# Performance work log

Measured on AMD Instinct MI355X. Metric: run time of the kernel, lower is better.

Reference implementation:

```python
import jax, jax.numpy as jnp
import numpy as np

H = 1024
B, S = 4, 2048
SCALE = 1.0 / np.sqrt(H)  # single-head: head_dim == hidden_dim


def setup_inputs() -> dict:
    key = jax.random.key(0)
    k1, k2, k3, k4 = jax.random.split(key, 4)
    inp = jax.random.normal(k1, (B, S, H), dtype=jnp.float32)
    # nn.Linear(h, h, bias=False) weights, stored [out, in]
    wq = jax.random.normal(k2, (H, H), dtype=jnp.float32) / np.sqrt(H)
    wk = jax.random.normal(k3, (H, H), dtype=jnp.float32) / np.sqrt(H)
    wv = jax.random.normal(k4, (H, H), dtype=jnp.float32) / np.sqrt(H)
    # causal mask, broadcast over batch: 1 = attend, 0 = masked
    attention_mask = jnp.broadcast_to(
        jnp.tril(jnp.ones((S, S), dtype=jnp.int32)), (B, S, S))
    return {"input": inp, "attention_mask": attention_mask,
            "wq": wq, "wk": wk, "wv": wv}


def reference(input, attention_mask, wq, wk, wv):
    # Linear: x @ W^T
    Q = jnp.einsum('bsh,oh->bso', input, wq)
    K = jnp.einsum('bsh,oh->bso', input, wk)
    V = jnp.einsum('bsh,oh->bso', input, wv)
    scores = jnp.einsum('bqh,bkh->bqk', Q, K) * SCALE  # [B,S,S]
    neg_inf = jnp.asarray(-jnp.inf, dtype=scores.dtype)
    scores = jnp.where(attention_mask == 0, neg_inf, scores)
    attn = jax.nn.softmax(scores, axis=-1)
    # dropout prob = 0.0 (eval): identity
    return jnp.einsum('bqk,bkh->bqh', attn, V)
```

## Files before the change

### kernel.cpp

```cpp
#include <hip/hip_runtime.h>
#include <hip/hip_bf16.h>
#include <stdint.h>

typedef __attribute__((ext_vector_type(8))) short short8;
typedef __attribute__((ext_vector_type(4))) float f32x4;
typedef __attribute__((ext_vector_type(4))) float fvec4;
typedef __attribute__((ext_vector_type(4))) unsigned short us4;

#define DEV static __device__ __forceinline__

constexpr int Hn = 1024;
constexpr int Bn = 4;
constexpr int Sn = 2048;
constexpr float SCALE_F = 0.03125f;
constexpr float LOG2E_F = 1.4426950408889634f;
constexpr float CEXP = SCALE_F * LOG2E_F;
constexpr int PTILES = 136;

DEV unsigned short f2bf(float f) {
  union { float f; unsigned u; } c; c.f = f;
  unsigned r = c.u + 0x7fffu + ((c.u >> 16) & 1u);
  return (unsigned short)(r >> 16);
}

DEV void gload16(const void* g, void* l) {
  __builtin_amdgcn_global_load_lds(
      (const __attribute__((address_space(1))) void*)g,
      (__attribute__((address_space(3))) void*)l, 16, 0, 0);
}

#define VMCNT(n) asm volatile("s_waitcnt vmcnt(" #n ")" ::: "memory")
#define LGKM0()  asm volatile("s_waitcnt lgkmcnt(0)" ::: "memory")
#define BAR()    asm volatile("s_barrier" ::: "memory")

DEV int swz_wg(int bid, int n) {
  const int q = n >> 3, r = n & 7, x = bid & 7, o = bid >> 3;
  return (x < r ? x * (q + 1) : r * (q + 1) + (x - r) * q) + o;
}

__global__ __launch_bounds__(256) void cvt_kernel(
    const float* __restrict__ x, const float* __restrict__ wq,
    const float* __restrict__ wk, const float* __restrict__ wv,
    unsigned short* __restrict__ xb, unsigned short* __restrict__ wb,
    float* __restrict__ lz) {
  if (blockIdx.x == 0) {
    f32x4 z = {0.f, 0.f, 0.f, 0.f};
    for (int i = threadIdx.x; i < Bn * Sn / 4; i += 256) ((f32x4*)lz)[i] = z;
  }
  const int NX4 = Bn * Sn * Hn / 4;
  const int NW4 = Hn * Hn / 4;
  const int total = NX4 + 3 * NW4;
  for (int i = blockIdx.x * 256 + threadIdx.x; i < total; i += gridDim.x * 256) {
    const fvec4* s; us4* d; int j;
    if (i < NX4)                { s = (const fvec4*)x;  d = (us4*)xb;             j = i; }
    else if (i < NX4 + NW4)     { s = (const fvec4*)wq; d = (us4*)wb;             j = i - NX4; }
    else if (i < NX4 + 2 * NW4) { s = (const fvec4*)wk; d = (us4*)(wb + Hn * Hn); j = i - NX4 - NW4; }
    else                        { s = (const fvec4*)wv; d = (us4*)(wb + 2 * Hn * Hn); j = i - NX4 - 2 * NW4; }
    fvec4 v = s[j];
    us4 o;
    o[0] = f2bf(v[0]); o[1] = f2bf(v[1]); o[2] = f2bf(v[2]); o[3] = f2bf(v[3]);
    d[j] = o;
  }
}

#define MFMA16(H, V, B) do {                                                     \
  __builtin_amdgcn_s_setprio(1);                                                 \
  _Pragma("unroll") for (int m_ = 0; m_ < 4; m_++)                               \
  _Pragma("unroll") for (int n_ = 0; n_ < 2; n_++)                               \
  _Pragma("unroll") for (int ks_ = 0; ks_ < 2; ks_++)                            \
    acc[H][V][m_][n_] = __builtin_amdgcn_mfma_f32_16x16x32_bf16(                 \
        afr[m_][ks_], (B)[n_][ks_], acc[H][V][m_][n_], 0, 0, 0);                 \
  __builtin_amdgcn_s_setprio(0);                                                 \
  __builtin_amdgcn_sched_barrier(0);                                             \
} while (0)

template <int MODE>
__global__ __launch_bounds__(512, 2) void gemm256_kernel(
    const unsigned short* __restrict__ A, int lda, int64_t a_bstride,
    const unsigned short* __restrict__ Bm, int ldb, int64_t b_bstride,
    unsigned short* __restrict__ C0, unsigned short* __restrict__ C1,
    float* __restrict__ lsum, int n_split, int ldc, int bm_mod, int K) {
  __shared__ __attribute__((aligned(16))) unsigned short LDSm[8][8192];
  char* lds = (char*)LDSm;
  const int tid = threadIdx.x, lane = tid & 63, wave = tid >> 6;
  const int wr = wave >> 2, wc = wave & 3;
  const int ln15 = lane & 15, hi = lane >> 4;

  int bm, bn, zl = 0;
  const int wg = swz_wg(blockIdx.x, gridDim.x);
  if (MODE == 0) { bm = wg % bm_mod; bn = wg / bm_mod; }
  else {
    zl = wg / 36;
    const int t = wg - zl * 36;
    bm = (int)((sqrtf(8.f * t + 1.f) - 1.f) * 0.5f);
    if (bm * (bm + 1) / 2 > t) bm--;
    if ((bm + 1) * (bm + 2) / 2 <= t) bm++;
    bn = t - bm * (bm + 1) / 2;
  }
  const unsigned short* Ab = A + (int64_t)zl * a_bstride;
  const unsigned short* Bb = Bm + (int64_t)zl * b_bstride;

  const int srow = tid >> 3;
  const int kch = ((tid & 7) ^ (srow & 7)) << 3;
  const unsigned short* Ag = Ab + (int64_t)(bm * 256 + srow) * lda + kch;
  const unsigned short* Bg = Bb + (int64_t)(bn * 256 + srow) * ldb + kch;
  const int dst_off = tid * 16;

  auto stageA = [&](int half, int t, int buf) {
    const unsigned short* s = Ag + (int64_t)(half * 128) * lda + (t << 6);
    char* d = lds + ((buf * 4 + half) << 14) + dst_off;
    gload16(s, d);
    gload16(s + (int64_t)64 * lda, d + 8192);
  };
  auto stageB = [&](int half, int t, int buf) {
    const unsigned short* s = Bg + (int64_t)(half * 128) * ldb + (t << 6);
    char* d = lds + ((buf * 4 + 2 + half) << 14) + dst_off;
    gload16(s, d);
    gload16(s + (int64_t)64 * ldb, d + 8192);
  };
  auto rdA = [&](int buf, int half, int rr, int ks) -> short8 {
    return *(const short8*)(lds + ((buf * 4 + half) << 14) + rr * 128 +
                            (((ks << 6) + (hi << 4)) ^ ((rr & 7) << 4)));
  };
  auto rdB = [&](int buf, int half, int rr, int ks) -> short8 {
    return *(const short8*)(lds + ((buf * 4 + 2 + half) << 14) + rr * 128 +
                            (((ks << 6) + (hi << 4)) ^ ((rr & 7) << 4)));
  };

  f32x4 acc[2][2][4][2];
#pragma unroll
  for (int h = 0; h < 2; h++)
#pragma unroll
    for (int v = 0; v < 2; v++)
#pragma unroll
      for (int m = 0; m < 4; m++)
#pragma unroll
        for (int n = 0; n < 2; n++) acc[h][v][m][n] = (f32x4){0.f, 0.f, 0.f, 0.f};

  short8 afr[4][2], b0r[2][2], b1r[2][2];

  stageA(0, 0, 0); stageB(0, 0, 0); stageB(1, 0, 0); stageA(1, 0, 0);
  VMCNT(4);
  BAR();

  const int nkt = K >> 6;
  for (int t = 0; t < nkt; ++t) {
    const int buf = t & 1, nb2 = buf ^ 1;
    const bool st = (t + 1 < nkt);
#pragma unroll
    for (int m = 0; m < 4; m++) {
      afr[m][0] = rdA(buf, 0, wr * 64 + m * 16 + ln15, 0);
      afr[m][1] = rdA(buf, 0, wr * 64 + m * 16 + ln15, 1);
    }
#pragma unroll
    for (int n = 0; n < 2; n++) {
      b0r[n][0] = rdB(buf, 0, wc * 32 + n * 16 + ln15, 0);
      b0r[n][1] = rdB(buf, 0, wc * 32 + n * 16 + ln15, 1);
    }
    if (st) { stageA(0, t + 1, nb2); VMCNT(4); } else { VMCNT(2); }
    BAR(); LGKM0(); __builtin_amdgcn_sched_barrier(0);
    MFMA16(0, 0, b0r);
    BAR();
#pragma unroll
    for (int n = 0; n < 2; n++) {
      b1r[n][0] = rdB(buf, 1, wc * 32 + n * 16 + ln15, 0);
      b1r[n][1] = rdB(buf, 1, wc * 32 + n * 16 + ln15, 1);
    }
    if (st) { stageB(0, t + 1, nb2); VMCNT(4); } else { VMCNT(0); }
    BAR(); LGKM0(); __builtin_amdgcn_sched_barrier(0);
    MFMA16(0, 1, b1r);
    BAR();
#pragma unroll
    for (int m = 0; m < 4; m++) {
      afr[m][0] = rdA(buf, 1, wr * 64 + m * 16 + ln15, 0);
      afr[m][1] = rdA(buf, 1, wr * 64 + m * 16 + ln15, 1);
    }
    if (st) { stageB(1, t + 1, nb2); VMCNT(6); } else { VMCNT(0); }
    BAR(); LGKM0(); __builtin_amdgcn_sched_barrier(0);
    MFMA16(1, 0, b0r);
    BAR();
    if (st) { stageA(1, t + 1, nb2); VMCNT(4); } else { VMCNT(0); }
    BAR();
    MFMA16(1, 1, b1r);
    BAR();
  }

  if (MODE == 0) {
#pragma unroll
    for (int h = 0; h < 2; h++)
#pragma unroll
      for (int v = 0; v < 2; v++)
#pragma unroll
        for (int n = 0; n < 2; n++) {
          int cc = bn * 256 + v * 128 + wc * 32 + n * 16;
          unsigned short* cb = C0;
          if (cc >= n_split) { cb = C1; cc -= n_split; }
          cc += ln15;
#pragma unroll
          for (int m = 0; m < 4; m++) {
            const int r0 = bm * 256 + h * 128 + wr * 64 + m * 16 + hi * 4;
#pragma unroll
            for (int j = 0; j < 4; j++)
              cb[(int64_t)(r0 + j) * ldc + cc] = f2bf(acc[h][v][m][n][j]);
          }
        }
  } else {
    unsigned short* Pb = C0 + (int64_t)zl * (PTILES * 16384);
    float* lb = lsum + zl * Sn;
#pragma unroll
    for (int h = 0; h < 2; h++)
#pragma unroll
      for (int m = 0; m < 4; m++)
#pragma unroll
        for (int j = 0; j < 4; j++) {
          const int row = bm * 256 + h * 128 + wr * 64 + m * 16 + hi * 4 + j;
          const int tq = row >> 7;
          float s = 0.f;
#pragma unroll
          for (int v = 0; v < 2; v++)
#pragma unroll
            for (int n = 0; n < 2; n++) {
              const int col = bn * 256 + v * 128 + wc * 32 + n * 16 + ln15;
              const float p =
                  (col <= row) ? __builtin_amdgcn_exp2f(acc[h][v][m][n][j] * CEXP) : 0.f;
              s += p;
              const int tk = col >> 7;
              if (tk <= tq)
                Pb[((int64_t)(tq * (tq + 1) / 2 + tk) << 14) + ((row & 127) << 7) +
                   (col & 127)] = f2bf(p);
            }
          s += __shfl_xor(s, 1); s += __shfl_xor(s, 2);
          s += __shfl_xor(s, 4); s += __shfl_xor(s, 8);
          if (ln15 == 0) atomicAdd(&lb[row], s);
        }
  }
}

__global__ __launch_bounds__(256, 2) void pv_gemm_kernel(
    const unsigned short* __restrict__ Pp,
    const unsigned short* __restrict__ VTb,
    const float* __restrict__ l,
    float* __restrict__ Out) {
  const int xcd = blockIdx.x & 7;
  const int inner = blockIdx.x >> 3;
  const int bn = inner & 7;
  const int slot = inner >> 3;
  const int r = slot * 8 + xcd;
  const int bm = 15 - (r >> 2);
  const int b = r & 3;

  __shared__ __attribute__((aligned(16))) unsigned short As[2][128 * 64];
  __shared__ __attribute__((aligned(16))) unsigned short Bs[2][128 * 64];
  const int tid = threadIdx.x, lane = tid & 63, wave = tid >> 6;
  const int wr = wave >> 1, wc = wave & 1;
  const int ln15 = lane & 15, hi = lane >> 4;

  const int srow0 = wave * 8 + (lane >> 3);
  const int gch = (((lane & 7) ^ (srow0 & 7)) << 3);
  const unsigned short* Pbase = Pp + (int64_t)b * (PTILES * 16384) +
      ((int64_t)(bm * (bm + 1) / 2) << 14);
  const unsigned short* Vbase = VTb + (int64_t)(bn * 128) * (Bn * Sn) + (int64_t)b * Sn;

  auto stage = [&](int kt, int buf) {
    char* a = (char*)As[buf] + wave * 1024;
    char* bl = (char*)Bs[buf] + wave * 1024;
    const int64_t a_off = ((int64_t)(kt >> 1) << 14) + (kt & 1) * 64 + gch;
    const int64_t v_off = (int64_t)kt * 64 + gch;
#pragma unroll
    for (int j = 0; j < 4; ++j) {
      const int row = srow0 + j * 32;
      gload16(Pbase + a_off + ((int64_t)row << 7), a + j * 4096);
      gload16(Vbase + v_off + (int64_t)row * (Bn * Sn), bl + j * 4096);
    }
  };

  f32x4 acc[4][4];
#pragma unroll
  for (int m = 0; m < 4; m++)
#pragma unroll
    for (int n = 0; n < 4; n++) acc[m][n] = (f32x4){0.f, 0.f, 0.f, 0.f};

  const int nkt = (bm + 1) * 2;
  stage(0, 0);
  for (int kt = 0; kt < nkt; ++kt) {
    const int buf = kt & 1;
    if (kt + 1 < nkt) { stage(kt + 1, buf ^ 1); VMCNT(8); }
    else { VMCNT(0); }
    BAR();
    const char* Ap = (const char*)As[buf];
    const char* Bp = (const char*)Bs[buf];
    short8 af[4][2], bf[4][2];
#pragma unroll
    for (int m = 0; m < 4; m++) {
      const int rr = wr * 64 + m * 16 + ln15;
#pragma unroll
      for (int ks = 0; ks < 2; ks++)
        af[m][ks] = *(const short8*)(Ap + rr * 128 + (((ks << 6) + (hi << 4)) ^ ((rr & 7) << 4)));
    }
#pragma unroll
    for (int n = 0; n < 4; n++) {
      const int rr = wc * 64 + n * 16 + ln15;
#pragma unroll
      for (int ks = 0; ks < 2; ks++)
        bf[n][ks] = *(const short8*)(Bp + rr * 128 + (((ks << 6) + (hi << 4)) ^ ((rr & 7) << 4)));
    }
#pragma unroll
    for (int ks = 0; ks < 2; ks++)
#pragma unroll
      for (int m = 0; m < 4; m++)
#pragma unroll
        for (int n = 0; n < 4; n++)
          acc[m][n] = __builtin_amdgcn_mfma_f32_16x16x32_bf16(af[m][ks], bf[n][ks], acc[m][n], 0, 0, 0);
    BAR();
  }

#pragma unroll
  for (int m = 0; m < 4; m++) {
    const int r0 = bm * 128 + wr * 64 + m * 16 + hi * 4;
#pragma unroll
    for (int j = 0; j < 4; j++) {
      const int q = r0 + j;
      const float linv = 1.0f / l[(int64_t)b * Sn + q];
#pragma unroll
      for (int n = 0; n < 4; n++) {
        const int d = bn * 128 + wc * 64 + n * 16 + ln15;
        Out[(int64_t)b * Sn * Hn + (int64_t)q * Hn + d] = acc[m][n][j] * linv;
      }
    }
  }
}

extern "C" void kernel_launch(void* const* d_in, const int* in_sizes, int n_in,
                              void* d_out, int out_size, void* d_ws, size_t ws_size,
                              hipStream_t stream) {
  const float* x  = (const float*)d_in[0];
  const float* wq = (const float*)d_in[2];
  const float* wk = (const float*)d_in[3];
  const float* wv = (const float*)d_in[4];
  float* out = (float*)d_out;
  char* ws = (char*)d_ws;

  const int64_t MiB = 1ll << 20;
  unsigned short* xb = (unsigned short*)(ws);
  unsigned short* wb = (unsigned short*)(ws + 16 * MiB);
  unsigned short* Pp = (unsigned short*)(ws);
  float* l           = (float*)(ws + 22 * MiB);
  unsigned short* Qb = (unsigned short*)(ws + 23 * MiB);
  unsigned short* Kb = (unsigned short*)(ws + 39 * MiB);
  unsigned short* VT = (unsigned short*)(ws + 55 * MiB);

  cvt_kernel<<<2048, 256, 0, stream>>>(x, wq, wk, wv, xb, wb, l);
  gemm256_kernel<0><<<256, 512, 0, stream>>>(
      xb, 1024, 0, wb, 1024, 0, Qb, Kb, nullptr, 1024, 1024, 32, 1024);
  gemm256_kernel<0><<<128, 512, 0, stream>>>(
      wb + 2 * 1024 * 1024, 1024, 0, xb, 1024, 0, VT, VT, nullptr, 1 << 30, 8192, 4, 1024);
  gemm256_kernel<1><<<144, 512, 0, stream>>>(
      Qb, 1024, (int64_t)Sn * Hn, Kb, 1024, (int64_t)Sn * Hn,
      Pp, nullptr, l, 1 << 30, 0, 0, 1024);
  pv_gemm_kernel<<<512, 256, 0, stream>>>(Pp, VT, l, out);
}
```

Measured before the change: 158.9 us.

## Use 128x128 tile GEMM kernel for V projection and causal QK^T scores

Adds a new 256-thread gemm128 kernel with simple double buffering and moves the V^T projection and the causal QK^T/exp stage onto it. The QK^T stage now launches one block per lower-triangular 128x128 tile (544 blocks) instead of 144 blocks on 256x256 tiles. This cuts wasted work above the diagonal and raises parallelism on the 256-CU part. In exchange it gives up the tuned 256-tile ping-pong pipeline and gets less operand reuse per block. The gemm256 kernel is reduced to the Q/K projection path only.

```diff
diff --git a/kernel.cpp b/kernel.cpp
--- a/kernel.cpp
+++ b/kernel.cpp
@@ -74,36 +74,24 @@
   __builtin_amdgcn_sched_barrier(0);                                             \
 } while (0)
 
-template <int MODE>
 __global__ __launch_bounds__(512, 2) void gemm256_kernel(
-    const unsigned short* __restrict__ A, int lda, int64_t a_bstride,
-    const unsigned short* __restrict__ Bm, int ldb, int64_t b_bstride,
+    const unsigned short* __restrict__ A, int lda,
+    const unsigned short* __restrict__ Bm, int ldb,
     unsigned short* __restrict__ C0, unsigned short* __restrict__ C1,
-    float* __restrict__ lsum, int n_split, int ldc, int bm_mod, int K) {
+    int n_split, int ldc, int bm_mod, int K) {
   __shared__ __attribute__((aligned(16))) unsigned short LDSm[8][8192];
   char* lds = (char*)LDSm;
   const int tid = threadIdx.x, lane = tid & 63, wave = tid >> 6;
   const int wr = wave >> 2, wc = wave & 3;
   const int ln15 = lane & 15, hi = lane >> 4;
 
-  int bm, bn, zl = 0;
   const int wg = swz_wg(blockIdx.x, gridDim.x);
-  if (MODE == 0) { bm = wg % bm_mod; bn = wg / bm_mod; }
-  else {
-    zl = wg / 36;
-    const int t = wg - zl * 36;
-    bm = (int)((sqrtf(8.f * t + 1.f) - 1.f) * 0.5f);
-    if (bm * (bm + 1) / 2 > t) bm--;
-    if ((bm + 1) * (bm + 2) / 2 <= t) bm++;
-    bn = t - bm * (bm + 1) / 2;
-  }
-  const unsigned short* Ab = A + (int64_t)zl * a_bstride;
-  const unsigned short* Bb = Bm + (int64_t)zl * b_bstride;
+  const int bm = wg % bm_mod, bn = wg / bm_mod;
 
   const int srow = tid >> 3;
   const int kch = ((tid & 7) ^ (srow & 7)) << 3;
-  const unsigned short* Ag = Ab + (int64_t)(bm * 256 + srow) * lda + kch;
-  const unsigned short* Bg = Bb + (int64_t)(bn * 256 + srow) * ldb + kch;
+  const unsigned short* Ag = A + (int64_t)(bm * 256 + srow) * lda + kch;
+  const unsigned short* Bg = Bm + (int64_t)(bn * 256 + srow) * ldb + kch;
   const int dst_off = tid * 16;
 
   auto stageA = [&](int half, int t, int buf) {
@@ -185,54 +173,148 @@
     BAR();
   }
 
+#pragma unroll
+  for (int h = 0; h < 2; h++)
+#pragma unroll
+    for (int v = 0; v < 2; v++)
+#pragma unroll
+      for (int n = 0; n < 2; n++) {
+        int cc = bn * 256 + v * 128 + wc * 32 + n * 16;
+        unsigned short* cb = C0;
+        if (cc >= n_split) { cb = C1; cc -= n_split; }
+        cc += ln15;
+#pragma unroll
+        for (int m = 0; m < 4; m++) {
+          const int r0 = bm * 256 + h * 128 + wr * 64 + m * 16 + hi * 4;
+#pragma unroll
+          for (int j = 0; j < 4; j++)
+            cb[(int64_t)(r0 + j) * ldc + cc] = f2bf(acc[h][v][m][n][j]);
+        }
+      }
+}
+
+template <int MODE>
+__global__ __launch_bounds__(256, 2) void gemm128_kernel(
+    const unsigned short* __restrict__ A, int lda, int64_t a_bstride,
+    const unsigned short* __restrict__ Bm, int ldb, int64_t b_bstride,
+    unsigned short* __restrict__ C0, unsigned short* __restrict__ C1,
+    float* __restrict__ lsum, int n_split, int ldc, int bm_mod, int K) {
+  __shared__ __attribute__((aligned(16))) unsigned short As[2][128 * 64];
+  __shared__ __attribute__((aligned(16))) unsigned short Bs[2][128 * 64];
+  const int tid = threadIdx.x, lane = tid & 63, wave = tid >> 6;
+  const int wr = wave >> 1, wc = wave & 1;
+  const int ln15 = lane & 15, hi = lane >> 4;
+
+  int bm, bn, zl = 0;
+  const int wg = swz_wg(blockIdx.x, gridDim.x);
+  if (MODE == 0) { bm = wg % bm_mod; bn = wg / bm_mod; }
+  else {
+    zl = wg / 136;
+    const int t = wg - zl * 136;
+    bm = (int)((sqrtf(8.f * t + 1.f) - 1.f) * 0.5f);
+    if (bm * (bm + 1) / 2 > t) bm--;
+    if ((bm + 1) * (bm + 2) / 2 <= t) bm++;
+    bn = t - bm * (bm + 1) / 2;
+  }
+  const unsigned short* Ab = A + (int64_t)zl * a_bstride;
+  const unsigned short* Bb = Bm + (int64_t)zl * b_bstride;
+
+  const int srow0 = wave * 8 + (lane >> 3);
+  const int gch = (((lane & 7) ^ (srow0 & 7)) << 3);
+  const unsigned short* Ag = Ab + (int64_t)(bm * 128 + srow0) * lda + gch;
+  const unsigned short* Bg = Bb + (int64_t)(bn * 128 + srow0) * ldb + gch;
+
+  auto stage = [&](int kt, int buf) {
+    char* a = (char*)As[buf] + wave * 1024;
+    char* bl = (char*)Bs[buf] + wave * 1024;
+    const int k0 = kt << 6;
+#pragma unroll
+    for (int j = 0; j < 4; ++j) {
+      gload16(Ag + (int64_t)(j * 32) * lda + k0, a + j * 4096);
+      gload16(Bg + (int64_t)(j * 32) * ldb + k0, bl + j * 4096);
+    }
+  };
+
+  f32x4 acc[4][4];
+#pragma unroll
+  for (int m = 0; m < 4; m++)
+#pragma unroll
+    for (int n = 0; n < 4; n++) acc[m][n] = (f32x4){0.f, 0.f, 0.f, 0.f};
+
+  const int nkt = K >> 6;
+  stage(0, 0);
+  for (int kt = 0; kt < nkt; ++kt) {
+    const int buf = kt & 1;
+    if (kt + 1 < nkt) { stage(kt + 1, buf ^ 1); VMCNT(8); }
+    else { VMCNT(0); }
+    BAR();
+    const char* Ap = (const char*)As[buf];
+    const char* Bp = (const char*)Bs[buf];
+    short8 af[4][2], bf[4][2];
+#pragma unroll
+    for (int m = 0; m < 4; m++) {
+      const int rr = wr * 64 + m * 16 + ln15;
+#pragma unroll
+      for (int ks = 0; ks < 2; ks++)
+        af[m][ks] = *(const short8*)(Ap + rr * 128 + (((ks << 6) + (hi << 4)) ^ ((rr & 7) << 4)));
+    }
+#pragma unroll
+    for (int n = 0; n < 4; n++) {
+      const int rr = wc * 64 + n * 16 + ln15;
+#pragma unroll
+      for (int ks = 0; ks < 2; ks++)
+        bf[n][ks] = *(const short8*)(Bp + rr * 128 + (((ks << 6) + (hi << 4)) ^ ((rr & 7) << 4)));
+    }
+#pragma unroll
+    for (int ks = 0; ks < 2; ks++)
+#pragma unroll
+      for (int m = 0; m < 4; m++)
+#pragma unroll
+        for (int n = 0; n < 4; n++)
+          acc[m][n] = __builtin_amdgcn_mfma_f32_16x16x32_bf16(af[m][ks], bf[n][ks], acc[m][n], 0, 0, 0);
+    BAR();
+  }
+
   if (MODE == 0) {
 #pragma unroll
-    for (int h = 0; h < 2; h++)
-#pragma unroll
-      for (int v = 0; v < 2; v++)
-#pragma unroll
-        for (int n = 0; n < 2; n++) {
-          int cc = bn * 256 + v * 128 + wc * 32 + n * 16;
-          unsigned short* cb = C0;
-          if (cc >= n_split) { cb = C1; cc -= n_split; }
-          cc += ln15;
-#pragma unroll
-          for (int m = 0; m < 4; m++) {
-            const int r0 = bm * 256 + h * 128 + wr * 64 + m * 16 + hi * 4;
-#pragma unroll
-            for (int j = 0; j < 4; j++)
-              cb[(int64_t)(r0 + j) * ldc + cc] = f2bf(acc[h][v][m][n][j]);
-          }
-        }
+    for (int n = 0; n < 4; n++) {
+      int cc = bn * 128 + wc * 64 + n * 16;
+      unsigned short* cb = C0;
+      if (cc >= n_split) { cb = C1; cc -= n_split; }
+      cc += ln15;
+#pragma unroll
+      for (int m = 0; m < 4; m++) {
+        const int r0 = bm * 128 + wr * 64 + m * 16 + hi * 4;
+#pragma unroll
+        for (int j = 0; j < 4; j++)
+          cb[(int64_t)(r0 + j) * ldc + cc] = f2bf(acc[m][n][j]);
+      }
+    }
   } else {
     unsigned short* Pb = C0 + (int64_t)zl * (PTILES * 16384);
     float* lb = lsum + zl * Sn;
-#pragma unroll
-    for (int h = 0; h < 2; h++)
-#pragma unroll
-      for (int m = 0; m < 4; m++)
-#pragma unroll
-        for (int j = 0; j < 4; j++) {
-          const int row = bm * 256 + h * 128 + wr * 64 + m * 16 + hi * 4 + j;
-          const int tq = row >> 7;
-          float s = 0.f;
-#pragma unroll
-          for (int v = 0; v < 2; v++)
-#pragma unroll
-            for (int n = 0; n < 2; n++) {
-              const int col = bn * 256 + v * 128 + wc * 32 + n * 16 + ln15;
-              const float p =
-                  (col <= row) ? __builtin_amdgcn_exp2f(acc[h][v][m][n][j] * CEXP) : 0.f;
-              s += p;
-              const int tk = col >> 7;
-              if (tk <= tq)
-                Pb[((int64_t)(tq * (tq + 1) / 2 + tk) << 14) + ((row & 127) << 7) +
-                   (col & 127)] = f2bf(p);
-            }
-          s += __shfl_xor(s, 1); s += __shfl_xor(s, 2);
-          s += __shfl_xor(s, 4); s += __shfl_xor(s, 8);
-          if (ln15 == 0) atomicAdd(&lb[row], s);
+    const int tile = bm * (bm + 1) / 2 + bn;
+#pragma unroll
+    for (int m = 0; m < 4; m++) {
+#pragma unroll
+      for (int j = 0; j < 4; j++) {
+        const int rl = wr * 64 + m * 16 + hi * 4 + j;
+        const int row = bm * 128 + rl;
+        float s = 0.f;
+#pragma unroll
+        for (int n = 0; n < 4; n++) {
+          const int cl = wc * 64 + n * 16 + ln15;
+          const int col = bn * 128 + cl;
+          const float p =
+              (col <= row) ? __builtin_amdgcn_exp2f(acc[m][n][j] * CEXP) : 0.f;
+          s += p;
+          Pb[((int64_t)tile << 14) + (rl << 7) + cl] = f2bf(p);
         }
+        s += __shfl_xor(s, 1); s += __shfl_xor(s, 2);
+        s += __shfl_xor(s, 4); s += __shfl_xor(s, 8);
+        if (ln15 == 0) atomicAdd(&lb[row], s);
+      }
+    }
   }
 }
 
@@ -350,12 +432,13 @@
   unsigned short* VT = (unsigned short*)(ws + 55 * MiB);
 
   cvt_kernel<<<2048, 256, 0, stream>>>(x, wq, wk, wv, xb, wb, l);
-  gemm256_kernel<0><<<256, 512, 0, stream>>>(
-      xb, 1024, 0, wb, 1024, 0, Qb, Kb, nullptr, 1024, 1024, 32, 1024);
-  gemm256_kernel<0><<<128, 512, 0, stream>>>(
-      wb + 2 * 1024 * 1024, 1024, 0, xb, 1024, 0, VT, VT, nullptr, 1 << 30, 8192, 4, 1024);
-  gemm256_kernel<1><<<144, 512, 0, stream>>>(
+  gemm256_kernel<<<256, 512, 0, stream>>>(
+      xb, 1024, wb, 1024, Qb, Kb, 1024, 1024, 32, 1024);
+  gemm128_kernel<0><<<512, 256, 0, stream>>>(
+      wb + 2 * 1024 * 1024, 1024, 0, xb, 1024, 0,
+      VT, VT, nullptr, 1 << 30, 8192, 8, 1024);
+  gemm128_kernel<1><<<544, 256, 0, stream>>>(
       Qb, 1024, (int64_t)Sn * Hn, Kb, 1024, (int64_t)Sn * Hn,
-      Pp, nullptr, l, 1 << 30, 0, 0, 1024);
+      Pp, nullptr, l, 1 << 30, Sn, 0, 1024);
   pv_gemm_kernel<<<512, 256, 0, stream>>>(Pp, VT, l, out);
 }
```

Measured after the change: 147.7 us. -7.1%, faster.

## Stage softmax P tile through LDS for vectorized stores and row sums

Applied to the files above, without the earlier changes.

The QK epilogue now writes exponentiated bf16 probabilities into shared memory and then emits coalesced 16-byte stores into the packed triangular P buffer. Row sums come from the stored bf16 values with a wider shuffle reduction, which cuts the number of atomics. The PV kernel's row-block ordering is changed so that the second half of the work is scheduled ascending instead of descending, rebalancing the causal workload. The cost is an extra barrier and LDS traffic, plus row sums that now come from rounded bf16 values.

```diff
diff --git a/kernel.cpp b/kernel.cpp
--- a/kernel.cpp
+++ b/kernel.cpp
@@ -21,6 +21,11 @@
   union { float f; unsigned u; } c; c.f = f;
   unsigned r = c.u + 0x7fffu + ((c.u >> 16) & 1u);
   return (unsigned short)(r >> 16);
+}
+
+DEV float bf2f(unsigned short b) {
+  union { unsigned u; float f; } c; c.u = ((unsigned)b) << 16;
+  return c.f;
 }
 
 DEV void gload16(const void* g, void* l) {
@@ -205,34 +210,46 @@
           }
         }
   } else {
-    unsigned short* Pb = C0 + (int64_t)zl * (PTILES * 16384);
+    unsigned short* Ps = (unsigned short*)LDSm;
+#pragma unroll
+    for (int h = 0; h < 2; h++)
+#pragma unroll
+      for (int v = 0; v < 2; v++)
+#pragma unroll
+        for (int m = 0; m < 4; m++)
+#pragma unroll
+          for (int n = 0; n < 2; n++)
+#pragma unroll
+            for (int j = 0; j < 4; j++) {
+              const int rl = h * 128 + wr * 64 + m * 16 + hi * 4 + j;
+              const int cl = v * 128 + wc * 32 + n * 16 + ln15;
+              const float p = ((bn * 256 + cl) <= (bm * 256 + rl))
+                                  ? __builtin_amdgcn_exp2f(acc[h][v][m][n][j] * CEXP)
+                                  : 0.f;
+              Ps[rl * 256 + cl] = f2bf(p);
+            }
+    __syncthreads();
+
+    unsigned short* Pz = C0 + (int64_t)zl * (PTILES * 16384);
     float* lb = lsum + zl * Sn;
 #pragma unroll
-    for (int h = 0; h < 2; h++)
-#pragma unroll
-      for (int m = 0; m < 4; m++)
-#pragma unroll
-        for (int j = 0; j < 4; j++) {
-          const int row = bm * 256 + h * 128 + wr * 64 + m * 16 + hi * 4 + j;
-          const int tq = row >> 7;
-          float s = 0.f;
-#pragma unroll
-          for (int v = 0; v < 2; v++)
-#pragma unroll
-            for (int n = 0; n < 2; n++) {
-              const int col = bn * 256 + v * 128 + wc * 32 + n * 16 + ln15;
-              const float p =
-                  (col <= row) ? __builtin_amdgcn_exp2f(acc[h][v][m][n][j] * CEXP) : 0.f;
-              s += p;
-              const int tk = col >> 7;
-              if (tk <= tq)
-                Pb[((int64_t)(tq * (tq + 1) / 2 + tk) << 14) + ((row & 127) << 7) +
-                   (col & 127)] = f2bf(p);
-            }
-          s += __shfl_xor(s, 1); s += __shfl_xor(s, 2);
-          s += __shfl_xor(s, 4); s += __shfl_xor(s, 8);
-          if (ln15 == 0) atomicAdd(&lb[row], s);
-        }
+    for (int i = 0; i < 16; ++i) {
+      const int idx = i * 4096 + tid * 8;
+      const int rl = idx >> 8, cl = idx & 255;
+      short8 v8 = *(const short8*)(Ps + idx);
+      const int tq = 2 * bm + (rl >> 7), tk = 2 * bn + (cl >> 7);
+      if (tk <= tq) {
+        unsigned short* dst = Pz + (((int64_t)(tq * (tq + 1) / 2 + tk)) << 14) +
+                              ((rl & 127) << 7) + (cl & 127);
+        *(short8*)dst = v8;
+      }
+      float s = 0.f;
+#pragma unroll
+      for (int e = 0; e < 8; ++e) s += bf2f((unsigned short)v8[e]);
+      s += __shfl_xor(s, 1); s += __shfl_xor(s, 2); s += __shfl_xor(s, 4);
+      s += __shfl_xor(s, 8); s += __shfl_xor(s, 16);
+      if ((lane & 31) == 0) atomicAdd(&lb[bm * 256 + rl], s);
+    }
   }
 }
 
@@ -246,7 +263,7 @@
   const int bn = inner & 7;
   const int slot = inner >> 3;
   const int r = slot * 8 + xcd;
-  const int bm = 15 - (r >> 2);
+  const int bm = (r < 32) ? (15 - (r >> 2)) : ((r - 32) >> 2);
   const int b = r & 3;
 
   __shared__ __attribute__((aligned(16))) unsigned short As[2][128 * 64];
@@ -353,7 +370,8 @@
   gemm256_kernel<0><<<256, 512, 0, stream>>>(
       xb, 1024, 0, wb, 1024, 0, Qb, Kb, nullptr, 1024, 1024, 32, 1024);
   gemm256_kernel<0><<<128, 512, 0, stream>>>(
-      wb + 2 * 1024 * 1024, 1024, 0, xb, 1024, 0, VT, VT, nullptr, 1 << 30, 8192, 4, 1024);
+      wb + 2 * 1024 * 1024, 1024, 0, xb, 1024, 0,
+      VT, VT, nullptr, 1 << 30, 8192, 4, 1024);
   gemm256_kernel<1><<<144, 512, 0, stream>>>(
       Qb, 1024, (int64_t)Sn * Hn, Kb, 1024, (int64_t)Sn * Hn,
       Pp, nullptr, l, 1 << 30, 0, 0, 1024);
```

Result: faster. 155.0 us (-2.5%).
